# Optimization experiments

Measured on AMD Instinct MI355X. Metric: run time of the kernel, lower is better.

## Reference

```python
import jax, jax.numpy as jnp
import numpy as np

_INF = -1e+30
N_HEAD, D_MODEL, D_HEAD = 16, 1024, 64
SCALE = 1.0 / float(np.sqrt(D_HEAD))
LN_EPS = 1e-5


def layer_norm(x, g, b):
    mu = jnp.mean(x, axis=-1, keepdims=True)
    var = jnp.mean(jnp.square(x - mu), axis=-1, keepdims=True)
    return (x - mu) * jax.lax.rsqrt(var + LN_EPS) * g + b


def setup_inputs() -> dict:
    key = jax.random.key(0)
    k_h, k_m, k_q, k_k, k_v, k_o = jax.random.split(key, 6)
    B, S = 2, 2048
    h = jax.random.normal(k_h, (B, S, D_MODEL), dtype=jnp.float32)
    attn_mask = jax.random.randint(k_m, (B, S), 0, 2, dtype=jnp.int32)
    # torch Linear weights: [out_features, in_features], init N(0, scale)
    q_w = jax.random.normal(k_q, (N_HEAD * D_HEAD, D_MODEL), dtype=jnp.float32) * SCALE
    k_w = jax.random.normal(k_k, (N_HEAD * D_HEAD, D_MODEL), dtype=jnp.float32) * SCALE
    v_w = jax.random.normal(k_v, (N_HEAD * D_HEAD, D_MODEL), dtype=jnp.float32) * SCALE
    o_w = jax.random.normal(k_o, (D_MODEL, N_HEAD * D_HEAD), dtype=jnp.float32) * SCALE
    ln_g = jnp.ones((D_MODEL,), dtype=jnp.float32)
    ln_b = jnp.zeros((D_MODEL,), dtype=jnp.float32)
    return {"h": h, "attn_mask": attn_mask, "q_w": q_w, "k_w": k_w,
            "v_w": v_w, "o_w": o_w, "ln_g": ln_g, "ln_b": ln_b}


def reference(h, attn_mask, q_w, k_w, v_w, o_w, ln_g, ln_b):
    B, S, _ = h.shape
    # mems=None -> c == h; pre_lnorm=False
    head_q = (h @ q_w.T).reshape(B, S, N_HEAD, D_HEAD)
    head_k = (h @ k_w.T).reshape(B, S, N_HEAD, D_HEAD)
    head_v = (h @ v_w.T).reshape(B, S, N_HEAD, D_HEAD)
    # scores [b, i(q), j(k), n]
    attn_score = jnp.einsum('bind,bjnd->bijn', head_q, head_k) * SCALE
    mask = (attn_mask == 0)[:, None, :, None]  # [b,1,j,1]
    attn_score = jnp.where(mask, _INF, attn_score)
    attn_prob = jax.nn.softmax(attn_score, axis=2)
    attn_vec = jnp.einsum('bijn,bjnd->bind', attn_prob, head_v)
    attn_vec = attn_vec.reshape(B, S, N_HEAD * D_HEAD)
    attn_out = attn_vec @ o_w.T
    output = h + attn_out  # dropout=0 -> identity
    return layer_norm(output, ln_g, ln_b)  # post-lnorm
```

## Files before the change

### kernel.cpp

```cpp
#include <hip/hip_runtime.h>
#include <hip/hip_bf16.h>

typedef __attribute__((ext_vector_type(8))) _Float16 hfx8;
typedef __attribute__((ext_vector_type(16))) float fx16;
typedef __attribute__((ext_vector_type(2))) __fp16 fp16x2;
typedef __attribute__((ext_vector_type(4))) float fx4;
typedef __attribute__((ext_vector_type(4))) unsigned short usx4;
typedef __attribute__((ext_vector_type(8))) unsigned short usx8;
typedef __attribute__((ext_vector_type(2))) unsigned int ux2;

#define LOG2E 1.44269504f

__device__ __forceinline__ unsigned short f2h(float f) {
  union { _Float16 h; unsigned short u; } c;
  c.h = (_Float16)f;
  return c.u;
}

__device__ __forceinline__ void async16(const void* g, void* l) {
  __builtin_amdgcn_global_load_lds(
      (const __attribute__((address_space(1))) void*)g,
      (__attribute__((address_space(3))) void*)l, 16, 0, 0);
}

__global__ __launch_bounds__(256)
void cvth(const float* __restrict__ s, unsigned short* __restrict__ d) {
  int i = (blockIdx.x * 256 + threadIdx.x) * 4;
  fx4 v = *(const fx4*)(s + i);
  usx4 o;
  o[0] = f2h(v[0]); o[1] = f2h(v[1]); o[2] = f2h(v[2]); o[3] = f2h(v[3]);
  *(usx4*)(d + i) = o;
}

__global__ __launch_bounds__(256)
void cvtw(const float* __restrict__ s0, const float* __restrict__ s1,
          const float* __restrict__ s2, const float* __restrict__ s3,
          unsigned short* __restrict__ d0, unsigned short* __restrict__ d1,
          unsigned short* __restrict__ d2, unsigned short* __restrict__ d3) {
  const int y = blockIdx.y;
  const float* s = (y == 0) ? s0 : (y == 1) ? s1 : (y == 2) ? s2 : s3;
  unsigned short* d = (y == 0) ? d0 : (y == 1) ? d1 : (y == 2) ? d2 : d3;
  int i = (blockIdx.x * 256 + threadIdx.x) * 4;
  fx4 v = *(const fx4*)(s + i);
  usx4 o;
  o[0] = f2h(v[0]); o[1] = f2h(v[1]); o[2] = f2h(v[2]); o[3] = f2h(v[3]);
  *(usx4*)(d + i) = o;
}

__global__ __launch_bounds__(256)
void maskscan(const int* __restrict__ mask, int* __restrict__ src, int* __restrict__ cnt) {
  const int b = blockIdx.x;
  const int tid = threadIdx.x;
  const int base = b * 2048 + tid * 8;
  int m[8];
  int s = 0;
#pragma unroll
  for (int e = 0; e < 8; ++e) { m[e] = mask[base + e] ? 1 : 0; s += m[e]; }
  const int lane = tid & 63, wv = tid >> 6;
  int inc = s;
#pragma unroll
  for (int off = 1; off < 64; off <<= 1) {
    int t = __shfl_up(inc, off);
    if (lane >= off) inc += t;
  }
  __shared__ int wsum[4];
  if (lane == 63) wsum[wv] = inc;
  __syncthreads();
  int wvoff = 0;
#pragma unroll
  for (int k = 0; k < 4; ++k)
    if (k < wv) wvoff += wsum[k];
  int run = wvoff + inc - s;
#pragma unroll
  for (int e = 0; e < 8; ++e) {
    if (m[e]) { src[b * 2048 + run] = tid * 8 + e; ++run; }
  }
  if (tid == 255) cnt[b] = run;
}

__global__ __launch_bounds__(256, 4)
void gemm_qkv(const unsigned short* __restrict__ A,
              const unsigned short* __restrict__ Wq,
              const unsigned short* __restrict__ Wk,
              const unsigned short* __restrict__ Wv,
              const int* __restrict__ src, const int* __restrict__ cnt,
              unsigned short* __restrict__ Qf, unsigned short* __restrict__ Kf,
              unsigned short* __restrict__ Vt) {
  __shared__ unsigned short As[128 * 64];
  __shared__ unsigned short Bs[128 * 64];
  const int tid = threadIdx.x;
  const int w = tid >> 6, ln = tid & 63;
  const int bid = blockIdx.x;
  const int wg = (bid & 7) * 96 + (bid >> 3);
  const int mt = wg & 31;
  const int by = wg >> 5;
  const int sel = by >> 3;
  const int nt = by & 7;
  const unsigned short* W = (sel == 0) ? Wq : ((sel == 1) ? Wk : Wv);
  const int n0 = nt * 128;
  const int wr = w >> 1, wc = w & 1;

  const int lr = ln >> 3;
  const int scg = (ln & 7) ^ lr;

  const int bI = mt >> 4;
  const int r0 = (mt & 15) * 128;
  int cnt_b = 0;
  const unsigned short* Arow[4];
  if (sel == 0) {
    const int m0 = mt * 128;
#pragma unroll
    for (int ii = 0; ii < 4; ++ii)
      Arow[ii] = A + (size_t)(m0 + w * 32 + ii * 8 + lr) * 1024 + scg * 8;
  } else {
    cnt_b = cnt[bI];
    if (r0 >= cnt_b) return;
#pragma unroll
    for (int ii = 0; ii < 4; ++ii) {
      int r = r0 + w * 32 + ii * 8 + lr;
      r = (r < cnt_b) ? r : (cnt_b - 1);
      Arow[ii] = A + (size_t)(bI * 2048 + src[bI * 2048 + r]) * 1024 + scg * 8;
    }
  }
  const unsigned short* Bsrc = W + (size_t)(n0 + w * 32 + lr) * 1024 + scg * 8;

  fx4 acc[4][4] = {};

  for (int kt = 0; kt < 16; ++kt) {
#pragma unroll
    for (int i = 0; i < 4; ++i) {
      async16(Arow[i] + kt * 64, &As[(w * 32 + i * 8) * 64]);
      async16(Bsrc + (size_t)i * 8 * 1024 + kt * 64, &Bs[(w * 32 + i * 8) * 64]);
    }
    __syncthreads();
#pragma unroll
    for (int kk = 0; kk < 2; ++kk) {
      const int kg = kk * 4 + (ln >> 4);
      hfx8 af[4], bfr[4];
#pragma unroll
      for (int mi = 0; mi < 4; ++mi) {
        int row = wr * 64 + mi * 16 + (ln & 15);
        af[mi] = *(const hfx8*)&As[row * 64 + ((kg ^ (row & 7)) * 8)];
      }
#pragma unroll
      for (int ni = 0; ni < 4; ++ni) {
        int row = wc * 64 + ni * 16 + (ln & 15);
        bfr[ni] = *(const hfx8*)&Bs[row * 64 + ((kg ^ (row & 7)) * 8)];
      }
#pragma unroll
      for (int mi = 0; mi < 4; ++mi)
#pragma unroll
        for (int ni = 0; ni < 4; ++ni)
          acc[mi][ni] = __builtin_amdgcn_mfma_f32_16x16x32_f16(af[mi], bfr[ni], acc[mi][ni], 0, 0, 0);
    }
    __syncthreads();
  }
  const int cb = n0 + wc * 64 + (ln & 15);
  const int rloc = wr * 64 + ((ln >> 4) << 2);
  if (sel == 0) {
    const int m0 = mt * 128;
#pragma unroll
    for (int mi = 0; mi < 4; ++mi)
#pragma unroll
      for (int ni = 0; ni < 4; ++ni)
#pragma unroll
        for (int j = 0; j < 4; ++j)
          Qf[(size_t)(m0 + rloc + mi * 16 + j) * 1024 + cb + ni * 16] = f2h(acc[mi][ni][j] * 0.125f);
  } else if (sel == 1) {
#pragma unroll
    for (int mi = 0; mi < 4; ++mi)
#pragma unroll
      for (int ni = 0; ni < 4; ++ni)
#pragma unroll
        for (int j = 0; j < 4; ++j)
          Kf[(size_t)(bI * 2048 + r0 + rloc + mi * 16 + j) * 1024 + cb + ni * 16] = f2h(acc[mi][ni][j]);
  } else {
#pragma unroll
    for (int mi = 0; mi < 4; ++mi)
#pragma unroll
      for (int ni = 0; ni < 4; ++ni) {
        int c = cb + ni * 16;
        int h2 = (c >> 6) & 15, d2 = c & 63;
        usx4 pk;
#pragma unroll
        for (int j = 0; j < 4; ++j) pk[j] = f2h(acc[mi][ni][j]);
        *(usx4*)&Vt[((size_t)(bI * 16 + h2) * 64 + d2) * 2048 + r0 + rloc + mi * 16] = pk;
      }
  }
}

__global__ __launch_bounds__(256, 4)
void gemm_o(const unsigned short* __restrict__ A,
            const unsigned short* __restrict__ W,
            float* __restrict__ O) {
  __shared__ unsigned short As[128 * 64];
  __shared__ unsigned short Bs[128 * 64];
  const int tid = threadIdx.x;
  const int w = tid >> 6, ln = tid & 63;
  const int mt = blockIdx.x, nt = blockIdx.y;
  const int m0 = mt * 128, n0 = nt * 128;
  const int wr = w >> 1, wc = w & 1;
  fx4 acc[4][4] = {};
  const int lr = ln >> 3;
  const int scg = (ln & 7) ^ lr;
  const unsigned short* Asrc = A + (size_t)(m0 + w * 32 + lr) * 1024 + scg * 8;
  const unsigned short* Bsrc = W + (size_t)(n0 + w * 32 + lr) * 1024 + scg * 8;

  for (int kt = 0; kt < 16; ++kt) {
#pragma unroll
    for (int i = 0; i < 4; ++i) {
      async16(Asrc + (size_t)i * 8 * 1024 + kt * 64, &As[(w * 32 + i * 8) * 64]);
      async16(Bsrc + (size_t)i * 8 * 1024 + kt * 64, &Bs[(w * 32 + i * 8) * 64]);
    }
    __syncthreads();
#pragma unroll
    for (int kk = 0; kk < 2; ++kk) {
      const int kg = kk * 4 + (ln >> 4);
      hfx8 af[4], bfr[4];
#pragma unroll
      for (int mi = 0; mi < 4; ++mi) {
        int row = wr * 64 + mi * 16 + (ln & 15);
        af[mi] = *(const hfx8*)&As[row * 64 + ((kg ^ (row & 7)) * 8)];
      }
#pragma unroll
      for (int ni = 0; ni < 4; ++ni) {
        int row = wc * 64 + ni * 16 + (ln & 15);
        bfr[ni] = *(const hfx8*)&Bs[row * 64 + ((kg ^ (row & 7)) * 8)];
      }
#pragma unroll
      for (int mi = 0; mi < 4; ++mi)
#pragma unroll
        for (int ni = 0; ni < 4; ++ni)
          acc[mi][ni] = __builtin_amdgcn_mfma_f32_16x16x32_f16(af[mi], bfr[ni], acc[mi][ni], 0, 0, 0);
    }
    __syncthreads();
  }
  const int cb = n0 + wc * 64 + (ln & 15);
  const int rb = m0 + wr * 64 + ((ln >> 4) << 2);
#pragma unroll
  for (int mi = 0; mi < 4; ++mi)
#pragma unroll
    for (int ni = 0; ni < 4; ++ni)
#pragma unroll
      for (int j = 0; j < 4; ++j)
        O[(size_t)(rb + mi * 16 + j) * 1024 + cb + ni * 16] = acc[mi][ni][j];
}

__global__ __launch_bounds__(256, 4)
void attn_fwd(const unsigned short* __restrict__ Qf,
              const unsigned short* __restrict__ Kf,
              const unsigned short* __restrict__ Vt,
              const int* __restrict__ cnt,
              unsigned short* __restrict__ Ov) {
  __shared__ __align__(16) unsigned short smem[16384];
  unsigned short* Ks = smem;
  unsigned short* Vs = smem + 8192;
  unsigned short* eb = smem;

  const int tid = threadIdx.x;
  const int w = tid >> 6, ln = tid & 63;
  const int bid = blockIdx.x;
  const int wg = (bid & 7) * 64 + (bid >> 3);
  const int qt = wg & 15, h = (wg >> 4) & 15, b = wg >> 8;
  const int l31 = ln & 31, h5 = ln >> 5;
  const int q = qt * 128 + w * 32 + l31;

  const int cnt_b = cnt[b];
  const int ntile = (cnt_b + 127) >> 7;

  hfx8 qb[4];
  {
    const unsigned short* qp = Qf + (size_t)(b * 2048 + q) * 1024 + h * 64 + h5 * 8;
    qb[0] = *(const hfx8*)(qp);
    qb[1] = *(const hfx8*)(qp + 16);
    qb[2] = *(const hfx8*)(qp + 32);
    qb[3] = *(const hfx8*)(qp + 48);
  }

  fx16 o0 = {}, o1 = {};
  float mrow = -INFINITY, lrow = 0.f;

#define A_STAGE(KT)                                                              \
  {                                                                              \
    _Pragma("unroll") for (int ii = 0; ii < 4; ++ii) {                           \
      int krow = w * 32 + ii * 8 + (ln >> 3);                                    \
      async16(Kf + ((size_t)(b * 2048 + (KT) * 128 + krow)) * 1024 + h * 64 +    \
                  (((ln & 7) ^ (ln >> 3)) * 8),                                  \
              &Ks[(w * 4 + ii) * 512]);                                          \
      int vswz = (ii * 4 + (ln >> 4)) & 7;                                       \
      int vrow = w * 16 + ii * 4 + (ln >> 4);                                    \
      async16(Vt + ((size_t)((b * 16 + h) * 64 + vrow)) * 2048 + (KT) * 128 +    \
                  (((ln & 15) ^ vswz) * 8),                                      \
              &Vs[(w * 4 + ii) * 512]);                                          \
    }                                                                            \
  }

  for (int kt = 0; kt < ntile; ++kt) {
    A_STAGE(kt);
    __syncthreads();
    const bool lastt = (kt == ntile - 1);

    fx16 sArr[4];
#pragma unroll
    for (int kb = 0; kb < 4; ++kb) {
      fx16 z = {};
      if (lastt) {
#pragma unroll
        for (int r = 0; r < 16; ++r) {
          int crow = (r & 3) + 8 * (r >> 2) + 4 * h5;
          int key = kt * 128 + kb * 32 + crow;
          z[r] = (key < cnt_b) ? 0.0f : -1e30f;
        }
      }
#pragma unroll
      for (int dc = 0; dc < 4; ++dc) {
        int row = kb * 32 + l31;
        int slot = (dc * 2 + h5) ^ (l31 & 7);
        hfx8 a = *(const hfx8*)&Ks[row * 64 + slot * 8];
        z = __builtin_amdgcn_mfma_f32_32x32x16_f16(a, qb[dc], z, 0, 0, 0);
      }
      sArr[kb] = z;
    }

    float tm = -INFINITY;
#pragma unroll
    for (int kb = 0; kb < 4; ++kb)
#pragma unroll
      for (int r = 0; r < 16; ++r) tm = fmaxf(tm, sArr[kb][r]);
    {
      auto t = __builtin_amdgcn_permlane32_swap(__float_as_uint(tm), __float_as_uint(tm), false, false);
      tm = fmaxf(__uint_as_float(t[0]), __uint_as_float(t[1]));
    }
    if (!__all(tm <= mrow + 8.0f)) {
      float mn = fmaxf(mrow, tm);
      float fac = exp2f((mrow - mn) * LOG2E);
      mrow = mn;
      lrow *= fac;
#pragma unroll
      for (int r = 0; r < 16; ++r) { o0[r] *= fac; o1[r] *= fac; }
    }
    const float nm2 = -mrow * LOG2E;
    float psum = 0.f;
    unsigned int pk[4][8];
#pragma unroll
    for (int kb = 0; kb < 4; ++kb) {
#pragma unroll
      for (int j = 0; j < 8; ++j) {
        float pa = exp2f(fmaf(sArr[kb][2 * j], LOG2E, nm2));
        float pb = exp2f(fmaf(sArr[kb][2 * j + 1], LOG2E, nm2));
        psum += pa + pb;
        union { fp16x2 h; unsigned int u; } rr;
        rr.h = __builtin_amdgcn_cvt_pkrtz(pa, pb);
        pk[kb][j] = rr.u;
      }
    }
    {
      auto t = __builtin_amdgcn_permlane32_swap(__float_as_uint(psum), __float_as_uint(psum), false, false);
      psum = __uint_as_float(t[0]) + __uint_as_float(t[1]);
    }
    lrow += psum;

#pragma unroll
    for (int kc = 0; kc < 8; ++kc) {
      const int kbq = kc >> 1;
      const int jb = (kc & 1) * 4;
      auto r0 = __builtin_amdgcn_permlane32_swap(pk[kbq][jb], pk[kbq][jb + 2], false, false);
      auto r1 = __builtin_amdgcn_permlane32_swap(pk[kbq][jb + 1], pk[kbq][jb + 3], false, false);
      union { unsigned int u[4]; hfx8 v; } B_;
      B_.u[0] = (unsigned int)r0[0];
      B_.u[1] = (unsigned int)r1[0];
      B_.u[2] = (unsigned int)r0[1];
      B_.u[3] = (unsigned int)r1[1];
      int slot = (kc * 2 + h5) ^ (l31 & 7);
      hfx8 va0 = *(const hfx8*)&Vs[(l31) * 128 + slot * 8];
      o0 = __builtin_amdgcn_mfma_f32_32x32x16_f16(va0, B_.v, o0, 0, 0, 0);
      hfx8 va1 = *(const hfx8*)&Vs[(32 + l31) * 128 + slot * 8];
      o1 = __builtin_amdgcn_mfma_f32_32x32x16_f16(va1, B_.v, o1, 0, 0, 0);
    }
    __syncthreads();
  }
#undef A_STAGE

  float inv = 1.0f / lrow;
  const int ql = w * 32 + l31;
#pragma unroll
  for (int db = 0; db < 2; ++db) {
#pragma unroll
    for (int r4 = 0; r4 < 4; ++r4) {
      float v0 = (db ? o1[4 * r4] : o0[4 * r4]) * inv;
      float v1 = (db ? o1[4 * r4 + 1] : o0[4 * r4 + 1]) * inv;
      float v2 = (db ? o1[4 * r4 + 2] : o0[4 * r4 + 2]) * inv;
      float v3 = (db ? o1[4 * r4 + 3] : o0[4 * r4 + 3]) * inv;
      union { fp16x2 h; unsigned int u; } pa_, pb_;
      pa_.h = __builtin_amdgcn_cvt_pkrtz(v0, v1);
      pb_.h = __builtin_amdgcn_cvt_pkrtz(v2, v3);
      ux2 tw; tw[0] = pa_.u; tw[1] = pb_.u;
      int d_base = db * 32 + 8 * r4 + 4 * h5;
      *(ux2*)&eb[ql * 88 + d_base] = tw;
    }
  }
  __syncthreads();
#pragma unroll
  for (int pass = 0; pass < 4; ++pass) {
    int idx = pass * 256 + tid;
    int qq = idx >> 3, slot = idx & 7;
    usx8 vv = *(const usx8*)&eb[qq * 88 + slot * 8];
    *(usx8*)&Ov[(size_t)(b * 2048 + qt * 128 + qq) * 1024 + h * 64 + slot * 8] = vv;
  }
}

__global__ __launch_bounds__(256)
void lnk(const float* __restrict__ h, const float* __restrict__ ao,
         const float* __restrict__ g, const float* __restrict__ bb,
         float* __restrict__ out) {
  const int row = blockIdx.x;
  const int tid = threadIdx.x;
  const size_t base = (size_t)row * 1024 + tid * 4;
  fx4 x = *(const fx4*)(h + base);
  fx4 a = *(const fx4*)(ao + base);
  x = x + a;
  float s = x[0] + x[1] + x[2] + x[3];
  float q = x[0] * x[0] + x[1] * x[1] + x[2] * x[2] + x[3] * x[3];
#pragma unroll
  for (int mm = 1; mm < 64; mm <<= 1) {
    s += __shfl_xor(s, mm);
    q += __shfl_xor(q, mm);
  }
  __shared__ float rs[4], rq[4];
  if ((tid & 63) == 0) { rs[tid >> 6] = s; rq[tid >> 6] = q; }
  __syncthreads();
  s = rs[0] + rs[1] + rs[2] + rs[3];
  q = rq[0] + rq[1] + rq[2] + rq[3];
  float mu = s * (1.0f / 1024.0f);
  float var = q * (1.0f / 1024.0f) - mu * mu;
  float rstd = rsqrtf(var + 1e-5f);
  fx4 gg = *(const fx4*)(g + tid * 4);
  fx4 bv = *(const fx4*)(bb + tid * 4);
  fx4 ov;
#pragma unroll
  for (int k = 0; k < 4; ++k) ov[k] = (x[k] - mu) * rstd * gg[k] + bv[k];
  *(fx4*)(out + base) = ov;
}

extern "C" void kernel_launch(void* const* d_in, const int* in_sizes, int n_in,
                              void* d_out, int out_size, void* d_ws, size_t ws_size,
                              hipStream_t stream) {
  const float* h = (const float*)d_in[0];
  const int* msk = (const int*)d_in[1];
  const float* qw = (const float*)d_in[2];
  const float* kw = (const float*)d_in[3];
  const float* vw = (const float*)d_in[4];
  const float* ow = (const float*)d_in[5];
  const float* lng = (const float*)d_in[6];
  const float* lnb = (const float*)d_in[7];
  float* out = (float*)d_out;
  char* ws = (char*)d_ws;

  const size_t MB = 1u << 20;
  unsigned short* h16 = (unsigned short*)(ws + 0 * MB);
  unsigned short* w16q = (unsigned short*)(ws + 8 * MB);
  unsigned short* w16k = (unsigned short*)(ws + 10 * MB);
  unsigned short* w16v = (unsigned short*)(ws + 12 * MB);
  unsigned short* w16o = (unsigned short*)(ws + 14 * MB);
  unsigned short* Qf  = (unsigned short*)(ws + 16 * MB);
  unsigned short* Kf  = (unsigned short*)(ws + 24 * MB);
  unsigned short* Vtb = (unsigned short*)(ws + 32 * MB);
  unsigned short* Av  = (unsigned short*)(ws + 40 * MB);
  float* Ao = (float*)(ws + 48 * MB);
  int* srcIdx = (int*)(ws + 48 * MB);
  int* cnt    = (int*)(ws + 48 * MB + 16384);

  cvth<<<dim3(4096), 256, 0, stream>>>(h, h16);
  cvtw<<<dim3(1024, 4), 256, 0, stream>>>(qw, kw, vw, ow, w16q, w16k, w16v, w16o);
  maskscan<<<dim3(2), 256, 0, stream>>>(msk, srcIdx, cnt);

  gemm_qkv<<<dim3(768), 256, 0, stream>>>(h16, w16q, w16k, w16v, srcIdx, cnt, Qf, Kf, Vtb);
  attn_fwd<<<dim3(512), 256, 0, stream>>>(Qf, Kf, Vtb, cnt, Av);
  gemm_o<<<dim3(32, 8), 256, 0, stream>>>(Av, w16o, Ao);
  lnk<<<dim3(4096), 256, 0, stream>>>(h, Ao, lng, lnb, out);
}
```

Measured before the change: 128.3 us.

## Split attention key range across two wave groups with in-block softmax merge

Doubles the attention block to 512 threads. Two groups of four waves each process half of the key tiles for the same 128 queries using separate LDS buffers, then merge their partial outputs and max/sum statistics through shared memory, flash-decoding style. This targets the 512-block grid underfilling the GPU by adding waves per query tile. The cost is doubled LDS per block, an extra merge phase with syncs, and one group idling when the tile count is odd. It also computes the row sum with a packed fp16 dot2 instead of fp32 adds.

```diff
diff --git a/kernel.cpp b/kernel.cpp
--- a/kernel.cpp
+++ b/kernel.cpp
@@ -246,27 +246,31 @@
         O[(size_t)(rb + mi * 16 + j) * 1024 + cb + ni * 16] = acc[mi][ni][j];
 }
 
-__global__ __launch_bounds__(256, 4)
+__global__ __launch_bounds__(512, 4)
 void attn_fwd(const unsigned short* __restrict__ Qf,
               const unsigned short* __restrict__ Kf,
               const unsigned short* __restrict__ Vt,
               const int* __restrict__ cnt,
               unsigned short* __restrict__ Ov) {
-  __shared__ __align__(16) unsigned short smem[16384];
-  unsigned short* Ks = smem;
-  unsigned short* Vs = smem + 8192;
+  __shared__ __align__(16) unsigned short smem[32768];
+  float* obufF = (float*)smem;
+  float* mlbuf = (float*)(smem + 16384);
   unsigned short* eb = smem;
 
   const int tid = threadIdx.x;
   const int w = tid >> 6, ln = tid & 63;
+  const int g = w >> 2, wsub = w & 3;
+  unsigned short* Ks = smem + g * 16384;
+  unsigned short* Vs = Ks + 8192;
   const int bid = blockIdx.x;
   const int wg = (bid & 7) * 64 + (bid >> 3);
   const int qt = wg & 15, h = (wg >> 4) & 15, b = wg >> 8;
   const int l31 = ln & 31, h5 = ln >> 5;
-  const int q = qt * 128 + w * 32 + l31;
+  const int q = qt * 128 + wsub * 32 + l31;
 
   const int cnt_b = cnt[b];
   const int ntile = (cnt_b + 127) >> 7;
+  const int nh0 = (ntile + 1) >> 1;
 
   hfx8 qb[4];
   {
@@ -279,130 +283,168 @@
 
   fx16 o0 = {}, o1 = {};
   float mrow = -INFINITY, lrow = 0.f;
+  const fp16x2 one2 = { (__fp16)1.0f, (__fp16)1.0f };
 
 #define A_STAGE(KT)                                                              \
   {                                                                              \
     _Pragma("unroll") for (int ii = 0; ii < 4; ++ii) {                           \
-      int krow = w * 32 + ii * 8 + (ln >> 3);                                    \
+      int krow = wsub * 32 + ii * 8 + (ln >> 3);                                 \
       async16(Kf + ((size_t)(b * 2048 + (KT) * 128 + krow)) * 1024 + h * 64 +    \
                   (((ln & 7) ^ (ln >> 3)) * 8),                                  \
-              &Ks[(w * 4 + ii) * 512]);                                          \
+              &Ks[(wsub * 4 + ii) * 512]);                                       \
       int vswz = (ii * 4 + (ln >> 4)) & 7;                                       \
-      int vrow = w * 16 + ii * 4 + (ln >> 4);                                    \
+      int vrow = wsub * 16 + ii * 4 + (ln >> 4);                                 \
       async16(Vt + ((size_t)((b * 16 + h) * 64 + vrow)) * 2048 + (KT) * 128 +    \
                   (((ln & 15) ^ vswz) * 8),                                      \
-              &Vs[(w * 4 + ii) * 512]);                                          \
+              &Vs[(wsub * 4 + ii) * 512]);                                       \
     }                                                                            \
   }
 
-  for (int kt = 0; kt < ntile; ++kt) {
-    A_STAGE(kt);
+  for (int i = 0; i < nh0; ++i) {
+    const int t = (g ? nh0 : 0) + i;
+    const bool active = t < (g ? ntile : nh0);
+    if (active) A_STAGE(t);
     __syncthreads();
-    const bool lastt = (kt == ntile - 1);
-
-    fx16 sArr[4];
-#pragma unroll
-    for (int kb = 0; kb < 4; ++kb) {
-      fx16 z = {};
-      if (lastt) {
-#pragma unroll
-        for (int r = 0; r < 16; ++r) {
-          int crow = (r & 3) + 8 * (r >> 2) + 4 * h5;
-          int key = kt * 128 + kb * 32 + crow;
-          z[r] = (key < cnt_b) ? 0.0f : -1e30f;
+    if (active) {
+      const bool lastt = (t == ntile - 1);
+
+      fx16 sArr[4];
+#pragma unroll
+      for (int kb = 0; kb < 4; ++kb) {
+        fx16 z = {};
+        if (lastt) {
+#pragma unroll
+          for (int r = 0; r < 16; ++r) {
+            int crow = (r & 3) + 8 * (r >> 2) + 4 * h5;
+            int key = t * 128 + kb * 32 + crow;
+            z[r] = (key < cnt_b) ? 0.0f : -1e30f;
+          }
         }
-      }
-#pragma unroll
-      for (int dc = 0; dc < 4; ++dc) {
-        int row = kb * 32 + l31;
-        int slot = (dc * 2 + h5) ^ (l31 & 7);
-        hfx8 a = *(const hfx8*)&Ks[row * 64 + slot * 8];
-        z = __builtin_amdgcn_mfma_f32_32x32x16_f16(a, qb[dc], z, 0, 0, 0);
-      }
-      sArr[kb] = z;
-    }
-
-    float tm = -INFINITY;
-#pragma unroll
-    for (int kb = 0; kb < 4; ++kb)
-#pragma unroll
-      for (int r = 0; r < 16; ++r) tm = fmaxf(tm, sArr[kb][r]);
-    {
-      auto t = __builtin_amdgcn_permlane32_swap(__float_as_uint(tm), __float_as_uint(tm), false, false);
-      tm = fmaxf(__uint_as_float(t[0]), __uint_as_float(t[1]));
-    }
-    if (!__all(tm <= mrow + 8.0f)) {
-      float mn = fmaxf(mrow, tm);
-      float fac = exp2f((mrow - mn) * LOG2E);
-      mrow = mn;
-      lrow *= fac;
-#pragma unroll
-      for (int r = 0; r < 16; ++r) { o0[r] *= fac; o1[r] *= fac; }
-    }
-    const float nm2 = -mrow * LOG2E;
-    float psum = 0.f;
-    unsigned int pk[4][8];
-#pragma unroll
-    for (int kb = 0; kb < 4; ++kb) {
-#pragma unroll
-      for (int j = 0; j < 8; ++j) {
-        float pa = exp2f(fmaf(sArr[kb][2 * j], LOG2E, nm2));
-        float pb = exp2f(fmaf(sArr[kb][2 * j + 1], LOG2E, nm2));
-        psum += pa + pb;
-        union { fp16x2 h; unsigned int u; } rr;
-        rr.h = __builtin_amdgcn_cvt_pkrtz(pa, pb);
-        pk[kb][j] = rr.u;
-      }
-    }
-    {
-      auto t = __builtin_amdgcn_permlane32_swap(__float_as_uint(psum), __float_as_uint(psum), false, false);
-      psum = __uint_as_float(t[0]) + __uint_as_float(t[1]);
-    }
-    lrow += psum;
-
-#pragma unroll
-    for (int kc = 0; kc < 8; ++kc) {
-      const int kbq = kc >> 1;
-      const int jb = (kc & 1) * 4;
-      auto r0 = __builtin_amdgcn_permlane32_swap(pk[kbq][jb], pk[kbq][jb + 2], false, false);
-      auto r1 = __builtin_amdgcn_permlane32_swap(pk[kbq][jb + 1], pk[kbq][jb + 3], false, false);
-      union { unsigned int u[4]; hfx8 v; } B_;
-      B_.u[0] = (unsigned int)r0[0];
-      B_.u[1] = (unsigned int)r1[0];
-      B_.u[2] = (unsigned int)r0[1];
-      B_.u[3] = (unsigned int)r1[1];
-      int slot = (kc * 2 + h5) ^ (l31 & 7);
-      hfx8 va0 = *(const hfx8*)&Vs[(l31) * 128 + slot * 8];
-      o0 = __builtin_amdgcn_mfma_f32_32x32x16_f16(va0, B_.v, o0, 0, 0, 0);
-      hfx8 va1 = *(const hfx8*)&Vs[(32 + l31) * 128 + slot * 8];
-      o1 = __builtin_amdgcn_mfma_f32_32x32x16_f16(va1, B_.v, o1, 0, 0, 0);
+#pragma unroll
+        for (int dc = 0; dc < 4; ++dc) {
+          int row = kb * 32 + l31;
+          int slot = (dc * 2 + h5) ^ (l31 & 7);
+          hfx8 a = *(const hfx8*)&Ks[row * 64 + slot * 8];
+          z = __builtin_amdgcn_mfma_f32_32x32x16_f16(a, qb[dc], z, 0, 0, 0);
+        }
+        sArr[kb] = z;
+      }
+
+      float tm = -INFINITY;
+#pragma unroll
+      for (int kb = 0; kb < 4; ++kb)
+#pragma unroll
+        for (int j = 0; j < 8; ++j)
+          tm = fmaxf(fmaxf(sArr[kb][2 * j], sArr[kb][2 * j + 1]), tm);
+      {
+        auto t2 = __builtin_amdgcn_permlane32_swap(__float_as_uint(tm), __float_as_uint(tm), false, false);
+        tm = fmaxf(__uint_as_float(t2[0]), __uint_as_float(t2[1]));
+      }
+      if (!__all(tm <= mrow + 8.0f)) {
+        float mn = fmaxf(mrow, tm);
+        float fac = exp2f((mrow - mn) * LOG2E);
+        mrow = mn;
+        lrow *= fac;
+#pragma unroll
+        for (int r = 0; r < 16; ++r) { o0[r] *= fac; o1[r] *= fac; }
+      }
+      const float nm2 = -mrow * LOG2E;
+      float psum = 0.f;
+      unsigned int pk[4][8];
+#pragma unroll
+      for (int kb = 0; kb < 4; ++kb) {
+#pragma unroll
+        for (int j = 0; j < 8; ++j) {
+          float pa = exp2f(fmaf(sArr[kb][2 * j], LOG2E, nm2));
+          float pb = exp2f(fmaf(sArr[kb][2 * j + 1], LOG2E, nm2));
+          union { fp16x2 h; unsigned int u; } rr;
+          rr.h = __builtin_amdgcn_cvt_pkrtz(pa, pb);
+          pk[kb][j] = rr.u;
+          psum = __builtin_amdgcn_fdot2(rr.h, one2, psum, false);
+        }
+      }
+      {
+        auto t2 = __builtin_amdgcn_permlane32_swap(__float_as_uint(psum), __float_as_uint(psum), false, false);
+        psum = __uint_as_float(t2[0]) + __uint_as_float(t2[1]);
+      }
+      lrow += psum;
+
+#pragma unroll
+      for (int kc = 0; kc < 8; ++kc) {
+        const int kbq = kc >> 1;
+        const int jb = (kc & 1) * 4;
+        auto r0 = __builtin_amdgcn_permlane32_swap(pk[kbq][jb], pk[kbq][jb + 2], false, false);
+        auto r1 = __builtin_amdgcn_permlane32_swap(pk[kbq][jb + 1], pk[kbq][jb + 3], false, false);
+        union { unsigned int u[4]; hfx8 v; } B_;
+        B_.u[0] = (unsigned int)r0[0];
+        B_.u[1] = (unsigned int)r1[0];
+        B_.u[2] = (unsigned int)r0[1];
+        B_.u[3] = (unsigned int)r1[1];
+        int slot = (kc * 2 + h5) ^ (l31 & 7);
+        hfx8 va0 = *(const hfx8*)&Vs[(l31) * 128 + slot * 8];
+        o0 = __builtin_amdgcn_mfma_f32_32x32x16_f16(va0, B_.v, o0, 0, 0, 0);
+        hfx8 va1 = *(const hfx8*)&Vs[(32 + l31) * 128 + slot * 8];
+        o1 = __builtin_amdgcn_mfma_f32_32x32x16_f16(va1, B_.v, o1, 0, 0, 0);
+      }
     }
     __syncthreads();
   }
 #undef A_STAGE
 
-  float inv = 1.0f / lrow;
-  const int ql = w * 32 + l31;
-#pragma unroll
-  for (int db = 0; db < 2; ++db) {
-#pragma unroll
-    for (int r4 = 0; r4 < 4; ++r4) {
-      float v0 = (db ? o1[4 * r4] : o0[4 * r4]) * inv;
-      float v1 = (db ? o1[4 * r4 + 1] : o0[4 * r4 + 1]) * inv;
-      float v2 = (db ? o1[4 * r4 + 2] : o0[4 * r4 + 2]) * inv;
-      float v3 = (db ? o1[4 * r4 + 3] : o0[4 * r4 + 3]) * inv;
-      union { fp16x2 h; unsigned int u; } pa_, pb_;
-      pa_.h = __builtin_amdgcn_cvt_pkrtz(v0, v1);
-      pb_.h = __builtin_amdgcn_cvt_pkrtz(v2, v3);
-      ux2 tw; tw[0] = pa_.u; tw[1] = pb_.u;
-      int d_base = db * 32 + 8 * r4 + 4 * h5;
-      *(ux2*)&eb[ql * 88 + d_base] = tw;
+  if (g == 1) {
+#pragma unroll
+    for (int r = 0; r < 16; ++r) {
+      int d = (r & 3) + 8 * (r >> 2) + 4 * h5;
+      obufF[(wsub * 64 + d) * 32 + l31] = o0[r];
+      obufF[(wsub * 64 + d + 32) * 32 + l31] = o1[r];
+    }
+    if (h5 == 0) {
+      mlbuf[(wsub * 32 + l31) * 2] = mrow;
+      mlbuf[(wsub * 32 + l31) * 2 + 1] = lrow;
     }
   }
   __syncthreads();
-#pragma unroll
-  for (int pass = 0; pass < 4; ++pass) {
-    int idx = pass * 256 + tid;
+  float inv = 0.f;
+  if (g == 0) {
+    float m1 = mlbuf[(wsub * 32 + l31) * 2];
+    float l1 = mlbuf[(wsub * 32 + l31) * 2 + 1];
+    float mN = fmaxf(mrow, m1);
+    float a0 = exp2f((mrow - mN) * LOG2E);
+    float a1 = exp2f((m1 - mN) * LOG2E);
+    float lC = lrow * a0 + l1 * a1;
+#pragma unroll
+    for (int r = 0; r < 16; ++r) {
+      int d = (r & 3) + 8 * (r >> 2) + 4 * h5;
+      o0[r] = o0[r] * a0 + obufF[(wsub * 64 + d) * 32 + l31] * a1;
+      o1[r] = o1[r] * a0 + obufF[(wsub * 64 + d + 32) * 32 + l31] * a1;
+    }
+    inv = 1.0f / lC;
+  }
+  __syncthreads();
+
+  if (g == 0) {
+    const int ql = wsub * 32 + l31;
+#pragma unroll
+    for (int db = 0; db < 2; ++db) {
+#pragma unroll
+      for (int r4 = 0; r4 < 4; ++r4) {
+        float v0 = (db ? o1[4 * r4] : o0[4 * r4]) * inv;
+        float v1 = (db ? o1[4 * r4 + 1] : o0[4 * r4 + 1]) * inv;
+        float v2 = (db ? o1[4 * r4 + 2] : o0[4 * r4 + 2]) * inv;
+        float v3 = (db ? o1[4 * r4 + 3] : o0[4 * r4 + 3]) * inv;
+        union { fp16x2 h; unsigned int u; } pa_, pb_;
+        pa_.h = __builtin_amdgcn_cvt_pkrtz(v0, v1);
+        pb_.h = __builtin_amdgcn_cvt_pkrtz(v2, v3);
+        ux2 tw; tw[0] = pa_.u; tw[1] = pb_.u;
+        int d_base = db * 32 + 8 * r4 + 4 * h5;
+        *(ux2*)&eb[ql * 88 + d_base] = tw;
+      }
+    }
+  }
+  __syncthreads();
+#pragma unroll
+  for (int pass = 0; pass < 2; ++pass) {
+    int idx = pass * 512 + tid;
     int qq = idx >> 3, slot = idx & 7;
     usx8 vv = *(const usx8*)&eb[qq * 88 + slot * 8];
     *(usx8*)&Ov[(size_t)(b * 2048 + qt * 128 + qq) * 1024 + h * 64 + slot * 8] = vv;
@@ -475,7 +517,7 @@
   maskscan<<<dim3(2), 256, 0, stream>>>(msk, srcIdx, cnt);
 
   gemm_qkv<<<dim3(768), 256, 0, stream>>>(h16, w16q, w16k, w16v, srcIdx, cnt, Qf, Kf, Vtb);
-  attn_fwd<<<dim3(512), 256, 0, stream>>>(Qf, Kf, Vtb, cnt, Av);
+  attn_fwd<<<dim3(512), 512, 0, stream>>>(Qf, Kf, Vtb, cnt, Av);
   gemm_o<<<dim3(32, 8), 256, 0, stream>>>(Av, w16o, Ao);
   lnk<<<dim3(4096), 256, 0, stream>>>(h, Ao, lng, lnb, out);
 }
```

Result: no change. 129.8 us (+1.2%).
